# Optimization experiments

Hardware: AMD Instinct MI355X
Metric: run time of the kernel (lower is better)

Reference implementation:

```python
import jax, jax.numpy as jnp
import numpy as np

B, N = 16, 300000          # batch, total anchors per image (all FPN levels concatenated)
PRE, POST = 2000, 1000     # num_pre_nms, num_post_nms
NMS_THR = 0.7
MIN_SIZE = 1e-3            # proposal_min_size
IMG_H, IMG_W = 800.0, 1333.0


def setup_inputs() -> dict:
    key = jax.random.key(0)
    k1, k2, k3, k4, k5, k6 = jax.random.split(key, 6)
    cls = jax.random.normal(k1, (B, N), dtype=jnp.float32)
    reg = jax.random.normal(k2, (B, N, 4), dtype=jnp.float32) * 0.1
    # anchors as valid (cx,cy,w,h)->(x1,y1,x2,y2) boxes inside the image
    cx = jax.random.uniform(k3, (B, N), dtype=jnp.float32, minval=0.0, maxval=IMG_W)
    cy = jax.random.uniform(k4, (B, N), dtype=jnp.float32, minval=0.0, maxval=IMG_H)
    w = jax.random.uniform(k5, (B, N), dtype=jnp.float32, minval=16.0, maxval=256.0)
    h = jax.random.uniform(k6, (B, N), dtype=jnp.float32, minval=16.0, maxval=256.0)
    anchors = jnp.stack([cx - 0.5 * w, cy - 0.5 * h, cx + 0.5 * w, cy + 0.5 * h], axis=-1)
    return {"cls": cls, "reg": reg, "anchors": anchors}


def _decode(anchor, reg):
    aw = anchor[:, 2] - anchor[:, 0]
    ah = anchor[:, 3] - anchor[:, 1]
    acx = anchor[:, 0] + 0.5 * aw
    acy = anchor[:, 1] + 0.5 * ah
    dx, dy, dw, dh = reg[:, 0], reg[:, 1], reg[:, 2], reg[:, 3]
    pcx = dx * aw + acx
    pcy = dy * ah + acy
    pw = jnp.exp(dw) * aw
    ph = jnp.exp(dh) * ah
    return jnp.stack([pcx - 0.5 * pw, pcy - 0.5 * ph, pcx + 0.5 * pw, pcy + 0.5 * ph], axis=-1)


def _iou_matrix(boxes):
    # boxes: [K,4] -> pairwise IoU [K,K]
    area = (boxes[:, 2] - boxes[:, 0]) * (boxes[:, 3] - boxes[:, 1])
    lt = jnp.maximum(boxes[:, None, :2], boxes[None, :, :2])
    rb = jnp.minimum(boxes[:, None, 2:], boxes[None, :, 2:])
    wh = jnp.clip(rb - lt, 0.0)
    inter = wh[..., 0] * wh[..., 1]
    union = area[:, None] + area[None, :] - inter
    return inter / jnp.maximum(union, 1e-8)


def _per_image(score, reg, anchor):
    # topk pre-NMS selection (lax.top_k returns score-descending order)
    top_s, idx = jax.lax.top_k(score, PRE)
    boxes = _decode(anchor[idx], reg[idx].reshape(-1, 4))
    # clip to image bounds
    bounds = jnp.array([IMG_W, IMG_H, IMG_W, IMG_H], dtype=boxes.dtype)
    boxes = jnp.clip(boxes, 0.0, bounds)
    # remove small boxes (mask instead of dynamic removal)
    w = boxes[:, 2] - boxes[:, 0]
    h = boxes[:, 3] - boxes[:, 1]
    valid = (w >= MIN_SIZE) & (h >= MIN_SIZE)
    s = jnp.where(valid, top_s, -jnp.inf)
    order = jnp.argsort(-s)  # score-descending, invalid last
    boxes = boxes[order]
    valid = valid[order]
    # greedy NMS: iterate highest-score-first, suppress later boxes with IoU > thr
    iou = _iou_matrix(boxes)
    rng = jnp.arange(PRE)
    def body(i, keep):
        sup = (iou[i] > NMS_THR) & keep[i]
        return keep & jnp.logical_not(sup & (rng > i))
    keep = jax.lax.fori_loop(0, PRE, body, valid)
    # gather kept boxes (score order preserved), pad with zeros past count
    sel = jnp.argsort(jnp.logical_not(keep), stable=True)[:POST]
    return boxes[sel] * keep[sel][:, None].astype(boxes.dtype)


def reference(cls, reg, anchors):
    # [B, POST, 4] proposals per image (zero-padded where fewer than POST kept)
    return jax.vmap(_per_image)(cls, reg, anchors)
```

## Files before the change

kernel.cpp:

```cpp
#include <hip/hip_runtime.h>

#define NB 16
#define NN 300000
#define PRE 2000
#define POST 1000

typedef unsigned long long ull;

static const size_t OFF_HIST1   = 0;
static const size_t OFF_HIST2   = 65536;
static const size_t OFF_HIST3   = 196608;
static const size_t OFF_CANDCNT = 327680;
static const size_t OFF_EQCNT   = 327936;
static const size_t OFF_BITMAP  = 328192;
static const size_t OFF_B1      = 332288;
static const size_t OFF_NEED1   = 332544;
static const size_t OFF_B2      = 332800;
static const size_t OFF_NEED2   = 333056;
static const size_t OFF_B3      = 333312;
static const size_t OFF_NEED3   = 333568;
static const size_t OFF_NVALID  = 333824;
static const size_t ZERO_BYTES  = 334080;
static const size_t OFF_CAND    = 334080;
static const size_t OFF_EQBUF   = 465152;
static const size_t OFF_KEYS    = 989440;
static const size_t OFF_BOXTMP  = 1251584;
static const size_t OFF_SORTED  = 1775872;
static const size_t OFF_MASK    = 2287872;

__device__ __forceinline__ unsigned f2u(float f){
  unsigned b = __float_as_uint(f);
  return (b & 0x80000000u) ? ~b : (b | 0x80000000u);
}

#define H1REP 8
#define H1STRIDE 1025
__global__ void k_hist1(const float* __restrict__ cls, unsigned* __restrict__ hist){
  __shared__ unsigned h[H1REP * H1STRIDE];
  int img = blockIdx.y;
  for (int i = threadIdx.x; i < H1REP * H1STRIDE; i += blockDim.x) h[i] = 0;
  __syncthreads();
  const float* p = cls + (size_t)img * NN;
  int stride = gridDim.x * blockDim.x;
  unsigned rep = (threadIdx.x & (H1REP - 1)) * H1STRIDE;
  for (int i = blockIdx.x * blockDim.x + threadIdx.x; i < NN; i += stride)
    atomicAdd(&h[rep + (f2u(p[i]) >> 22)], 1u);
  __syncthreads();
  unsigned* g = hist + img * 1024;
  for (int i = threadIdx.x; i < 1024; i += blockDim.x){
    unsigned v = 0;
    for (int r = 0; r < H1REP; r++) v += h[r * H1STRIDE + i];
    if (v) atomicAdd(&g[i], v);
  }
}

__global__ void k_scan(const unsigned* __restrict__ hist, int bins,
                       const unsigned* __restrict__ tgt, unsigned K0,
                       unsigned* __restrict__ outBin, unsigned* __restrict__ outNeed){
  int img = blockIdx.x;
  int t = threadIdx.x;
  const unsigned* hh = hist + img * bins;
  unsigned K = tgt ? tgt[img] : K0;
  int per = bins >> 8;
  unsigned s = 0;
  for (int q = 0; q < per; q++) s += hh[bins - 1 - (t * per + q)];
  __shared__ unsigned arr[256];
  arr[t] = s;
  __syncthreads();
  for (int off = 1; off < 256; off <<= 1){
    unsigned v = (t >= off) ? arr[t - off] : 0u;
    __syncthreads();
    arr[t] += v;
    __syncthreads();
  }
  unsigned incl = arr[t], excl = incl - s;
  if (excl < K && K <= incl){
    unsigned c = excl;
    for (int q = 0; q < per; q++){
      int b = bins - 1 - (t * per + q);
      unsigned cnt = hh[b];
      if (c + cnt >= K){ outBin[img] = (unsigned)b; outNeed[img] = K - c; break; }
      c += cnt;
    }
  }
}

__global__ void k_hist2(const float* __restrict__ cls, const unsigned* __restrict__ b1,
                        unsigned* __restrict__ hist){
  int img = blockIdx.y;
  unsigned bb1 = b1[img];
  const float* p = cls + (size_t)img * NN;
  unsigned* g = hist + img * 2048;
  int stride = gridDim.x * blockDim.x;
  for (int i = blockIdx.x * blockDim.x + threadIdx.x; i < NN; i += stride){
    unsigned u = f2u(p[i]);
    if ((u >> 22) == bb1) atomicAdd(&g[(u >> 11) & 0x7FFu], 1u);
  }
}

__global__ void k_hist3(const float* __restrict__ cls, const unsigned* __restrict__ b1,
                        const unsigned* __restrict__ b2, unsigned* __restrict__ hist){
  int img = blockIdx.y;
  unsigned pref = (b1[img] << 11) | b2[img];
  const float* p = cls + (size_t)img * NN;
  unsigned* g = hist + img * 2048;
  int stride = gridDim.x * blockDim.x;
  for (int i = blockIdx.x * blockDim.x + threadIdx.x; i < NN; i += stride){
    unsigned u = f2u(p[i]);
    if ((u >> 11) == pref) atomicAdd(&g[u & 0x7FFu], 1u);
  }
}

__global__ void k_compact(const float* __restrict__ cls, const unsigned* __restrict__ b1,
                          const unsigned* __restrict__ b2, const unsigned* __restrict__ b3,
                          unsigned* __restrict__ cand, unsigned* __restrict__ candCnt,
                          unsigned* __restrict__ eqbuf, unsigned* __restrict__ eqCnt){
  __shared__ unsigned lc[1024];
  __shared__ unsigned le[256];
  __shared__ unsigned lcn, len_, baseC, baseE;
  int img = blockIdx.y;
  if (threadIdx.x == 0){ lcn = 0; len_ = 0; }
  __syncthreads();
  unsigned T = (b1[img] << 22) | (b2[img] << 11) | b3[img];
  const float* p = cls + (size_t)img * NN;
  int stride = gridDim.x * blockDim.x;
  for (int i = blockIdx.x * blockDim.x + threadIdx.x; i < NN; i += stride){
    unsigned u = f2u(p[i]);
    if (u > T){
      unsigned pos = atomicAdd(&lcn, 1u);
      if (pos < 1024u) lc[pos] = (unsigned)i;
      else { unsigned g = atomicAdd(&candCnt[img], 1u); if (g < 2048u) cand[img * 2048 + g] = (unsigned)i; }
    } else if (u == T){
      unsigned pos = atomicAdd(&len_, 1u);
      if (pos < 256u) le[pos] = (unsigned)i;
      else { unsigned g = atomicAdd(&eqCnt[img], 1u); if (g < 8192u) eqbuf[img * 8192 + g] = (unsigned)i; }
    }
  }
  __syncthreads();
  unsigned nc = lcn < 1024u ? lcn : 1024u;
  unsigned ne = len_ < 256u ? len_ : 256u;
  if (threadIdx.x == 0){
    if (nc) baseC = atomicAdd(&candCnt[img], nc);
    if (ne) baseE = atomicAdd(&eqCnt[img], ne);
  }
  __syncthreads();
  for (unsigned t = threadIdx.x; t < nc; t += blockDim.x){
    unsigned g = baseC + t;
    if (g < 2048u) cand[img * 2048 + g] = lc[t];
  }
  for (unsigned t = threadIdx.x; t < ne; t += blockDim.x){
    unsigned g = baseE + t;
    if (g < 8192u) eqbuf[img * 8192 + g] = le[t];
  }
}

__global__ void k_finalize(unsigned* __restrict__ cand, const unsigned* __restrict__ candCnt,
                           const unsigned* __restrict__ eqbuf, const unsigned* __restrict__ eqCnt,
                           const unsigned* __restrict__ need3){
  int img = blockIdx.x, tid = threadIdx.x;
  unsigned need = need3[img];
  unsigned ec = eqCnt[img]; if (ec > 8192u) ec = 8192u;
  unsigned base = candCnt[img];
  const unsigned* eq = eqbuf + img * 8192;
  unsigned* c = cand + img * 2048;
  if (need >= ec){
    for (unsigned t = tid; t < ec; t += 256) if (base + t < 2048u) c[base + t] = eq[t];
    return;
  }
  for (unsigned t = tid; t < ec; t += 256){
    unsigned v = eq[t], r = 0;
    for (unsigned s = 0; s < ec; s++) r += (eq[s] < v) ? 1u : 0u;
    if (r < need && base + r < 2048u) c[base + r] = v;
  }
}

__global__ void k_decode(const float* __restrict__ cls, const float* __restrict__ reg,
                         const float* __restrict__ anch, const unsigned* __restrict__ cand,
                         float* __restrict__ boxTmp, ull* __restrict__ keys,
                         unsigned* __restrict__ nvalid){
  int s = blockIdx.x * blockDim.x + threadIdx.x;
  if (s >= NB * 2048) return;
  int img = s >> 11, slot = s & 2047;
  ull key = 0ull;
  float4 box = make_float4(0.f, 0.f, 0.f, 0.f);
  bool counted = false;
  if (slot < PRE){
    unsigned i = cand[img * 2048 + slot];
    if (i < NN){
      size_t gi = (size_t)img * NN + i;
      float4 a = ((const float4*)anch)[gi];
      float4 r = ((const float4*)reg)[gi];
      float sc = cls[gi];
      float aw = a.z - a.x, ah = a.w - a.y;
      float acx = a.x + 0.5f * aw, acy = a.y + 0.5f * ah;
      float pcx = r.x * aw + acx, pcy = r.y * ah + acy;
      float pw = expf(r.z) * aw, ph = expf(r.w) * ah;
      float x1 = pcx - 0.5f * pw, y1 = pcy - 0.5f * ph;
      float x2 = pcx + 0.5f * pw, y2 = pcy + 0.5f * ph;
      x1 = fminf(fmaxf(x1, 0.f), 1333.f); x2 = fminf(fmaxf(x2, 0.f), 1333.f);
      y1 = fminf(fmaxf(y1, 0.f), 800.f);  y2 = fminf(fmaxf(y2, 0.f), 800.f);
      bool valid = ((x2 - x1) >= 0.001f) && ((y2 - y1) >= 0.001f);
      unsigned up = valid ? f2u(sc) : 0u;
      key = ((ull)up << 32) | (ull)(0xFFFFFFFFu - i);
      box = make_float4(x1, y1, x2, y2);
      counted = valid;
    }
  }
  keys[img * 2048 + slot] = key;
  ((float4*)boxTmp)[img * 2048 + slot] = box;
  ull bal = __ballot(counted);
  if ((threadIdx.x & 63) == 0 && bal)
    atomicAdd(&nvalid[img], (unsigned)__popcll(bal));
}

__global__ __launch_bounds__(256) void k_rank(const ull* __restrict__ keys,
                                              const float* __restrict__ boxTmp,
                                              float* __restrict__ sorted){
  __shared__ ull lk[2048];
  int img = blockIdx.y;
  int e = blockIdx.x * 256 + threadIdx.x;
  for (int t = threadIdx.x; t < 2048; t += 256) lk[t] = keys[img * 2048 + t];
  __syncthreads();
  ull me = lk[e];
  unsigned rank = 0;
  #pragma unroll 8
  for (int j = 0; j < 2048; j++) rank += (lk[j] > me) ? 1u : 0u;
  if (rank < PRE)
    ((float4*)sorted)[img * PRE + rank] = ((const float4*)boxTmp)[img * 2048 + e];
}

__global__ __launch_bounds__(512) void k_mask(const float* __restrict__ sorted,
                                              const unsigned* __restrict__ nvalid,
                                              ull* __restrict__ mask, ull* __restrict__ bitmap){
  __shared__ float4 bx[PRE];
  __shared__ float  ar[PRE];
  __shared__ unsigned rowflag[16];
  int img = blockIdx.y, tid = threadIdx.x;
  if (tid < 16) rowflag[tid] = 0;
  for (int i = tid; i < PRE; i += 512){
    float4 b = ((const float4*)sorted)[img * PRE + i];
    bx[i] = b;
    ar[i] = (b.z - b.x) * (b.w - b.y);
  }
  __syncthreads();
  int row = blockIdx.x * 16 + (tid >> 5);
  int w = tid & 31;
  float4 bi = bx[row];
  float ai = ar[row];
  int qlo = (row >= w) ? (((row - w) >> 5) + 1) : 0;
  int qhi = ((PRE - 1 - w) >> 5) + 1;
  ull m = 0;
  for (int q = qlo; q < qhi; q++){
    int j = (q << 5) + w;
    float4 bj = bx[j];
    float xx1 = fmaxf(bi.x, bj.x), yy1 = fmaxf(bi.y, bj.y);
    float xx2 = fminf(bi.z, bj.z), yy2 = fminf(bi.w, bj.w);
    float ww = fmaxf(xx2 - xx1, 0.f), hh = fmaxf(yy2 - yy1, 0.f);
    float inter = ww * hh;
    float uni = ai + ar[j] - inter;
    if (inter / fmaxf(uni, 1e-8f) > 0.7f) m |= (1ull << q);
  }
  mask[((size_t)(img * PRE + row)) * 32 + w] = m;
  if (m) atomicOr(&rowflag[tid >> 5], 1u);
  __syncthreads();
  if (tid < 16){
    int r = blockIdx.x * 16 + tid;
    if (rowflag[tid] && r < (int)nvalid[img])
      atomicOr(&bitmap[img * 32 + (r >> 6)], 1ull << (r & 63));
  }
}

#define CHR 48
__global__ __launch_bounds__(256) void k_nms(const ull* __restrict__ mask,
                                             const ull* __restrict__ bitmap,
                                             const unsigned* __restrict__ nvalid,
                                             const float* __restrict__ sorted,
                                             float* __restrict__ out){
  __shared__ unsigned rowsLds[2048];
  __shared__ unsigned cntw[32];
  __shared__ unsigned wbaseS[32];
  __shared__ int mcountS, mpS;
  __shared__ ull cacheD[2][CHR * 32];
  __shared__ ull keepP[32];
  __shared__ ull keepLin[32];
  __shared__ unsigned cntArr[32], preArr[32];
  int img = blockIdx.x, tid = threadIdx.x;
  int lane = tid & 63, wave = tid >> 6;

  if (tid < 32) cntw[tid] = (unsigned)__popcll(bitmap[img * 32 + tid]);
  __syncthreads();
  if (tid == 0){
    unsigned s = 0;
    for (int w0 = 0; w0 < 32; w0++){ wbaseS[w0] = s; s += cntw[w0]; }
    mcountS = (int)s;
    mpS = ((int)s + CHR - 1) / CHR * CHR;
  }
  __syncthreads();
  int m = mcountS, mp = mpS;
  if (tid < 32){
    ull bits = bitmap[img * 32 + tid];
    unsigned pos = wbaseS[tid];
    int base_i = tid * 64;
    while (bits){
      int b = __ffsll((long long)bits) - 1;
      rowsLds[pos++] = (unsigned)(base_i + b);
      bits &= bits - 1;
    }
  }
  for (int t = m + tid; t < mp; t += 256) rowsLds[t] = PRE - 1;
  __syncthreads();

  int nch = mp / CHR;
  ull remv = 0;
  const ull* mg = mask + (size_t)img * PRE * 32;

  if (nch > 0 && tid >= 64){
    int s = tid - 64;
    ull v[8];
    #pragma unroll
    for (int k = 0; k < 8; k++){
      int t = k * 192 + s;
      unsigned rr = rowsLds[t >> 5];
      v[k] = mg[(size_t)rr * 32 + (t & 31)];
    }
    #pragma unroll
    for (int k = 0; k < 8; k++) cacheD[0][k * 192 + s] = v[k];
  }
  __syncthreads();

  for (int c = 0; c < nch; c++){
    int cb = c & 1;
    if (tid >= 64){
      if (c + 1 < nch){
        int q0n = (c + 1) * CHR;
        int s = tid - 64;
        ull v[8];
        #pragma unroll
        for (int k = 0; k < 8; k++){
          int t = k * 192 + s;
          unsigned rr = rowsLds[q0n + (t >> 5)];
          v[k] = mg[(size_t)rr * 32 + (t & 31)];
        }
        #pragma unroll
        for (int k = 0; k < 8; k++) cacheD[cb ^ 1][k * 192 + s] = v[k];
      }
    } else {
      const ull* cbuf = cacheD[cb];
      const int q0 = c * CHR;
      ull cur[8]; unsigned ci[8];
      #pragma unroll
      for (int k = 0; k < 8; k++){
        ci[k] = rowsLds[q0 + k];
        cur[k] = cbuf[(k << 5) | (lane & 31)];
      }
      #pragma unroll
      for (int g = 0; g < 6; g++){
        ull nxt[8]; unsigned ni[8];
        if (g < 5){
          #pragma unroll
          for (int k = 0; k < 8; k++){
            int lq = (g + 1) * 8 + k;
            ni[k] = rowsLds[q0 + lq];
            nxt[k] = cbuf[(lq << 5) | (lane & 31)];
          }
        }
        #pragma unroll
        for (int k = 0; k < 8; k++){
          unsigned i = ci[k];
          unsigned bit = ((unsigned)(remv >> (i >> 5))) & 1u;
          int sup = (lane == (int)(i & 31)) && bit;
          if (!__any(sup)) remv |= cur[k];
        }
        if (g < 5){
          #pragma unroll
          for (int k = 0; k < 8; k++){ cur[k] = nxt[k]; ci[k] = ni[k]; }
        }
      }
    }
    __syncthreads();
  }

  int nv = (int)nvalid[img];
  if (wave == 0 && lane < 32){
    int cnt2 = (nv > lane) ? (((nv - 1 - lane) >> 5) + 1) : 0;
    ull vm = (cnt2 >= 64) ? ~0ull : ((1ull << cnt2) - 1ull);
    keepP[lane] = (~remv) & vm;
  }
  __syncthreads();
  if (tid < 32){
    ull lin = 0;
    for (int kk = 0; kk < 64; kk++)
      lin |= ((keepP[kk & 31] >> (2 * tid + (kk >> 5))) & 1ull) << kk;
    keepLin[tid] = lin;
    cntArr[tid] = (unsigned)__popcll(lin);
  }
  __syncthreads();
  if (tid < 32){
    unsigned pre = 0;
    for (int w0 = 0; w0 < tid; w0++) pre += cntArr[w0];
    preArr[tid] = pre;
  }
  __syncthreads();
  for (int i = tid; i < PRE; i += 256){
    int w0 = i >> 6, b = i & 63;
    ull kw = keepLin[w0];
    if ((kw >> b) & 1ull){
      unsigned rank = preArr[w0] + (unsigned)__popcll(kw & ((1ull << b) - 1ull));
      if (rank < POST)
        ((float4*)out)[img * POST + rank] = ((const float4*)sorted)[img * PRE + i];
    }
  }
}

extern "C" void kernel_launch(void* const* d_in, const int* in_sizes, int n_in,
                              void* d_out, int out_size, void* d_ws, size_t ws_size,
                              hipStream_t stream){
  const float* cls  = (const float*)d_in[0];
  const float* reg  = (const float*)d_in[1];
  const float* anch = (const float*)d_in[2];
  float* out = (float*)d_out;
  char* ws = (char*)d_ws;

  unsigned* hist1   = (unsigned*)(ws + OFF_HIST1);
  unsigned* hist2   = (unsigned*)(ws + OFF_HIST2);
  unsigned* hist3   = (unsigned*)(ws + OFF_HIST3);
  unsigned* candCnt = (unsigned*)(ws + OFF_CANDCNT);
  unsigned* eqCnt   = (unsigned*)(ws + OFF_EQCNT);
  ull*      bitmap  = (ull*)     (ws + OFF_BITMAP);
  unsigned* b1      = (unsigned*)(ws + OFF_B1);
  unsigned* need1   = (unsigned*)(ws + OFF_NEED1);
  unsigned* b2      = (unsigned*)(ws + OFF_B2);
  unsigned* need2   = (unsigned*)(ws + OFF_NEED2);
  unsigned* b3      = (unsigned*)(ws + OFF_B3);
  unsigned* need3   = (unsigned*)(ws + OFF_NEED3);
  unsigned* nvalid  = (unsigned*)(ws + OFF_NVALID);
  unsigned* cand    = (unsigned*)(ws + OFF_CAND);
  unsigned* eqbuf   = (unsigned*)(ws + OFF_EQBUF);
  ull*      keys    = (ull*)     (ws + OFF_KEYS);
  float*    boxTmp  = (float*)   (ws + OFF_BOXTMP);
  float*    sorted  = (float*)   (ws + OFF_SORTED);
  ull*      mask    = (ull*)     (ws + OFF_MASK);

  hipMemsetAsync(ws, 0, ZERO_BYTES, stream);
  hipMemsetAsync(d_out, 0, (size_t)out_size * sizeof(float), stream);

  k_hist1<<<dim3(64, NB), 256, 0, stream>>>(cls, hist1);
  k_scan <<<NB, 256, 0, stream>>>(hist1, 1024, (const unsigned*)nullptr, 2000u, b1, need1);
  k_hist2<<<dim3(64, NB), 256, 0, stream>>>(cls, b1, hist2);
  k_scan <<<NB, 256, 0, stream>>>(hist2, 2048, need1, 0u, b2, need2);
  k_hist3<<<dim3(64, NB), 256, 0, stream>>>(cls, b1, b2, hist3);
  k_scan <<<NB, 256, 0, stream>>>(hist3, 2048, need2, 0u, b3, need3);
  k_compact<<<dim3(64, NB), 256, 0, stream>>>(cls, b1, b2, b3, cand, candCnt, eqbuf, eqCnt);
  k_finalize<<<NB, 256, 0, stream>>>(cand, candCnt, eqbuf, eqCnt, need3);
  k_decode<<<(NB * 2048) / 256, 256, 0, stream>>>(cls, reg, anch, cand, boxTmp, keys, nvalid);
  k_rank<<<dim3(8, NB), 256, 0, stream>>>(keys, boxTmp, sorted);
  k_mask<<<dim3(PRE / 16, NB), 512, 0, stream>>>(sorted, nvalid, mask, bitmap);
  k_nms<<<NB, 256, 0, stream>>>(mask, bitmap, nvalid, sorted, out);
}
```

Baseline: 305.3 us.

## Replace three-pass radix select with single compaction of boundary bin plus in-block refinement

The top-k threshold search drops the second and third full passes over the 300k scores per image. A single compaction pass now writes strictly-above-bin indices and stashes boundary-bin (key, index) pairs into a buffer. One block per image then refines the threshold with two shared-memory histograms, resolves ties and decodes boxes, so the separate finalize and decode kernels go away. The output memset is replaced by zero-filling only the unused tail in the NMS kernel. The risk is that the boundary buffer is capped at 8192 entries and the fused select runs only 16 blocks, which serializes the decode work.

```diff
diff --git a/kernel.cpp b/kernel.cpp
--- a/kernel.cpp
+++ b/kernel.cpp
@@ -8,25 +8,19 @@
 typedef unsigned long long ull;
 
 static const size_t OFF_HIST1   = 0;
-static const size_t OFF_HIST2   = 65536;
-static const size_t OFF_HIST3   = 196608;
-static const size_t OFF_CANDCNT = 327680;
-static const size_t OFF_EQCNT   = 327936;
-static const size_t OFF_BITMAP  = 328192;
-static const size_t OFF_B1      = 332288;
-static const size_t OFF_NEED1   = 332544;
-static const size_t OFF_B2      = 332800;
-static const size_t OFF_NEED2   = 333056;
-static const size_t OFF_B3      = 333312;
-static const size_t OFF_NEED3   = 333568;
-static const size_t OFF_NVALID  = 333824;
-static const size_t ZERO_BYTES  = 334080;
-static const size_t OFF_CAND    = 334080;
-static const size_t OFF_EQBUF   = 465152;
-static const size_t OFF_KEYS    = 989440;
-static const size_t OFF_BOXTMP  = 1251584;
-static const size_t OFF_SORTED  = 1775872;
-static const size_t OFF_MASK    = 2287872;
+static const size_t OFF_CANDCNT = 65536;
+static const size_t OFF_BINCNT  = 65792;
+static const size_t OFF_B1      = 66048;
+static const size_t OFF_NEED1   = 66304;
+static const size_t OFF_NVALID  = 66560;
+static const size_t OFF_BITMAP  = 66816;
+static const size_t ZERO_BYTES  = 70912;
+static const size_t OFF_CAND    = 70912;
+static const size_t OFF_KEYS    = 201984;
+static const size_t OFF_BOXTMP  = 464128;
+static const size_t OFF_SORTED  = 988416;
+static const size_t OFF_MASK    = 1500416;
+static const size_t OFF_BINBUF  = OFF_MASK;
 
 __device__ __forceinline__ unsigned f2u(float f){
   unsigned b = __float_as_uint(f);
@@ -55,12 +49,12 @@
 }
 
 __global__ void k_scan(const unsigned* __restrict__ hist, int bins,
-                       const unsigned* __restrict__ tgt, unsigned K0,
+                       unsigned K0,
                        unsigned* __restrict__ outBin, unsigned* __restrict__ outNeed){
   int img = blockIdx.x;
   int t = threadIdx.x;
   const unsigned* hh = hist + img * bins;
-  unsigned K = tgt ? tgt[img] : K0;
+  unsigned K = K0;
   int per = bins >> 8;
   unsigned s = 0;
   for (int q = 0; q < per; q++) s += hh[bins - 1 - (t * per + q)];
@@ -85,132 +79,192 @@
   }
 }
 
-__global__ void k_hist2(const float* __restrict__ cls, const unsigned* __restrict__ b1,
-                        unsigned* __restrict__ hist){
+__global__ void k_compactA(const float* __restrict__ cls, const unsigned* __restrict__ b1,
+                           unsigned* __restrict__ cand, unsigned* __restrict__ candCnt,
+                           ull* __restrict__ binbuf, unsigned* __restrict__ binCnt){
+  __shared__ unsigned lc[1024];
+  __shared__ ull lb[512];
+  __shared__ unsigned lcn, lbn, baseC, baseB;
   int img = blockIdx.y;
+  if (threadIdx.x == 0){ lcn = 0; lbn = 0; }
+  __syncthreads();
   unsigned bb1 = b1[img];
-  const float* p = cls + (size_t)img * NN;
-  unsigned* g = hist + img * 2048;
-  int stride = gridDim.x * blockDim.x;
-  for (int i = blockIdx.x * blockDim.x + threadIdx.x; i < NN; i += stride){
-    unsigned u = f2u(p[i]);
-    if ((u >> 22) == bb1) atomicAdd(&g[(u >> 11) & 0x7FFu], 1u);
-  }
-}
-
-__global__ void k_hist3(const float* __restrict__ cls, const unsigned* __restrict__ b1,
-                        const unsigned* __restrict__ b2, unsigned* __restrict__ hist){
-  int img = blockIdx.y;
-  unsigned pref = (b1[img] << 11) | b2[img];
-  const float* p = cls + (size_t)img * NN;
-  unsigned* g = hist + img * 2048;
-  int stride = gridDim.x * blockDim.x;
-  for (int i = blockIdx.x * blockDim.x + threadIdx.x; i < NN; i += stride){
-    unsigned u = f2u(p[i]);
-    if ((u >> 11) == pref) atomicAdd(&g[u & 0x7FFu], 1u);
-  }
-}
-
-__global__ void k_compact(const float* __restrict__ cls, const unsigned* __restrict__ b1,
-                          const unsigned* __restrict__ b2, const unsigned* __restrict__ b3,
-                          unsigned* __restrict__ cand, unsigned* __restrict__ candCnt,
-                          unsigned* __restrict__ eqbuf, unsigned* __restrict__ eqCnt){
-  __shared__ unsigned lc[1024];
-  __shared__ unsigned le[256];
-  __shared__ unsigned lcn, len_, baseC, baseE;
-  int img = blockIdx.y;
-  if (threadIdx.x == 0){ lcn = 0; len_ = 0; }
-  __syncthreads();
-  unsigned T = (b1[img] << 22) | (b2[img] << 11) | b3[img];
   const float* p = cls + (size_t)img * NN;
   int stride = gridDim.x * blockDim.x;
   for (int i = blockIdx.x * blockDim.x + threadIdx.x; i < NN; i += stride){
     unsigned u = f2u(p[i]);
-    if (u > T){
+    unsigned top = u >> 22;
+    if (top > bb1){
       unsigned pos = atomicAdd(&lcn, 1u);
       if (pos < 1024u) lc[pos] = (unsigned)i;
       else { unsigned g = atomicAdd(&candCnt[img], 1u); if (g < 2048u) cand[img * 2048 + g] = (unsigned)i; }
-    } else if (u == T){
-      unsigned pos = atomicAdd(&len_, 1u);
-      if (pos < 256u) le[pos] = (unsigned)i;
-      else { unsigned g = atomicAdd(&eqCnt[img], 1u); if (g < 8192u) eqbuf[img * 8192 + g] = (unsigned)i; }
+    } else if (top == bb1){
+      ull e = ((ull)u << 32) | (unsigned)i;
+      unsigned pos = atomicAdd(&lbn, 1u);
+      if (pos < 512u) lb[pos] = e;
+      else { unsigned g = atomicAdd(&binCnt[img], 1u); if (g < 8192u) binbuf[img * 8192 + g] = e; }
     }
   }
   __syncthreads();
   unsigned nc = lcn < 1024u ? lcn : 1024u;
-  unsigned ne = len_ < 256u ? len_ : 256u;
+  unsigned nb = lbn < 512u ? lbn : 512u;
   if (threadIdx.x == 0){
     if (nc) baseC = atomicAdd(&candCnt[img], nc);
-    if (ne) baseE = atomicAdd(&eqCnt[img], ne);
+    if (nb) baseB = atomicAdd(&binCnt[img], nb);
   }
   __syncthreads();
   for (unsigned t = threadIdx.x; t < nc; t += blockDim.x){
     unsigned g = baseC + t;
     if (g < 2048u) cand[img * 2048 + g] = lc[t];
   }
-  for (unsigned t = threadIdx.x; t < ne; t += blockDim.x){
-    unsigned g = baseE + t;
-    if (g < 8192u) eqbuf[img * 8192 + g] = le[t];
-  }
-}
-
-__global__ void k_finalize(unsigned* __restrict__ cand, const unsigned* __restrict__ candCnt,
-                           const unsigned* __restrict__ eqbuf, const unsigned* __restrict__ eqCnt,
-                           const unsigned* __restrict__ need3){
+  for (unsigned t = threadIdx.x; t < nb; t += blockDim.x){
+    unsigned g = baseB + t;
+    if (g < 8192u) binbuf[img * 8192 + g] = lb[t];
+  }
+}
+
+__global__ __launch_bounds__(256) void k_select(const float* __restrict__ cls,
+                                                const float* __restrict__ reg,
+                                                const float* __restrict__ anch,
+                                                unsigned* __restrict__ cand,
+                                                const unsigned* __restrict__ candCnt,
+                                                const ull* __restrict__ binbuf,
+                                                const unsigned* __restrict__ binCnt,
+                                                const unsigned* __restrict__ need1,
+                                                float* __restrict__ boxTmp,
+                                                ull* __restrict__ keys,
+                                                unsigned* __restrict__ nvalid){
+  __shared__ unsigned hist[2048];
+  __shared__ unsigned arr[256];
+  __shared__ unsigned b2s, need2s, b3s, need3s;
+  __shared__ unsigned tiePos[1024];
+  __shared__ unsigned wcnt, tieCnt;
   int img = blockIdx.x, tid = threadIdx.x;
-  unsigned need = need3[img];
-  unsigned ec = eqCnt[img]; if (ec > 8192u) ec = 8192u;
+  unsigned bc = binCnt[img]; if (bc > 8192u) bc = 8192u;
   unsigned base = candCnt[img];
-  const unsigned* eq = eqbuf + img * 8192;
-  unsigned* c = cand + img * 2048;
-  if (need >= ec){
-    for (unsigned t = tid; t < ec; t += 256) if (base + t < 2048u) c[base + t] = eq[t];
-    return;
-  }
+  unsigned need = need1[img];
+  const ull* bb = binbuf + img * 8192;
+
+  if (tid == 0){ wcnt = 0; tieCnt = 0; b2s = 0; need2s = 0; b3s = 0; need3s = 0; }
+  for (int i = tid; i < 2048; i += 256) hist[i] = 0;
+  __syncthreads();
+  for (unsigned t = tid; t < bc; t += 256){
+    unsigned u = (unsigned)(bb[t] >> 32);
+    atomicAdd(&hist[(u >> 11) & 0x7FFu], 1u);
+  }
+  __syncthreads();
+  {
+    unsigned s = 0;
+    for (int q = 0; q < 8; q++) s += hist[2047 - (tid * 8 + q)];
+    arr[tid] = s; __syncthreads();
+    for (int off = 1; off < 256; off <<= 1){
+      unsigned v = (tid >= off) ? arr[tid - off] : 0u;
+      __syncthreads(); arr[tid] += v; __syncthreads();
+    }
+    unsigned incl = arr[tid], excl = incl - s;
+    if (excl < need && need <= incl){
+      unsigned c = excl;
+      for (int q = 0; q < 8; q++){
+        int b = 2047 - (tid * 8 + q);
+        unsigned cnt = hist[b];
+        if (c + cnt >= need){ b2s = (unsigned)b; need2s = need - c; break; }
+        c += cnt;
+      }
+    }
+  }
+  __syncthreads();
+  unsigned b2 = b2s, need2 = need2s;
+  for (int i = tid; i < 2048; i += 256) hist[i] = 0;
+  __syncthreads();
+  for (unsigned t = tid; t < bc; t += 256){
+    unsigned u = (unsigned)(bb[t] >> 32);
+    if (((u >> 11) & 0x7FFu) == b2) atomicAdd(&hist[u & 0x7FFu], 1u);
+  }
+  __syncthreads();
+  {
+    unsigned s = 0;
+    for (int q = 0; q < 8; q++) s += hist[2047 - (tid * 8 + q)];
+    arr[tid] = s; __syncthreads();
+    for (int off = 1; off < 256; off <<= 1){
+      unsigned v = (tid >= off) ? arr[tid - off] : 0u;
+      __syncthreads(); arr[tid] += v; __syncthreads();
+    }
+    unsigned incl = arr[tid], excl = incl - s;
+    if (excl < need2 && need2 <= incl){
+      unsigned c = excl;
+      for (int q = 0; q < 8; q++){
+        int b = 2047 - (tid * 8 + q);
+        unsigned cnt = hist[b];
+        if (c + cnt >= need2){ b3s = (unsigned)b; need3s = need2 - c; break; }
+        c += cnt;
+      }
+    }
+  }
+  __syncthreads();
+  unsigned b3 = b3s, need3 = need3s;
+  for (unsigned t = tid; t < bc; t += 256){
+    ull e = bb[t];
+    unsigned u = (unsigned)(e >> 32);
+    unsigned mid = (u >> 11) & 0x7FFu, low = u & 0x7FFu;
+    bool take = (mid > b2) || (mid == b2 && low > b3);
+    bool tie  = (mid == b2) && (low == b3);
+    if (take){
+      unsigned p = atomicAdd(&wcnt, 1u);
+      unsigned g = base + p;
+      if (g < 2048u) cand[img * 2048 + g] = (unsigned)(e & 0xFFFFFFFFull);
+    } else if (tie){
+      unsigned p = atomicAdd(&tieCnt, 1u);
+      if (p < 1024u) tiePos[p] = t;
+    }
+  }
+  __syncthreads();
+  unsigned above = wcnt;
+  unsigned ec = tieCnt; if (ec > 1024u) ec = 1024u;
   for (unsigned t = tid; t < ec; t += 256){
-    unsigned v = eq[t], r = 0;
-    for (unsigned s = 0; s < ec; s++) r += (eq[s] < v) ? 1u : 0u;
-    if (r < need && base + r < 2048u) c[base + r] = v;
-  }
-}
-
-__global__ void k_decode(const float* __restrict__ cls, const float* __restrict__ reg,
-                         const float* __restrict__ anch, const unsigned* __restrict__ cand,
-                         float* __restrict__ boxTmp, ull* __restrict__ keys,
-                         unsigned* __restrict__ nvalid){
-  int s = blockIdx.x * blockDim.x + threadIdx.x;
-  if (s >= NB * 2048) return;
-  int img = s >> 11, slot = s & 2047;
-  ull key = 0ull;
-  float4 box = make_float4(0.f, 0.f, 0.f, 0.f);
-  bool counted = false;
-  if (slot < PRE){
-    unsigned i = cand[img * 2048 + slot];
-    if (i < NN){
-      size_t gi = (size_t)img * NN + i;
-      float4 a = ((const float4*)anch)[gi];
-      float4 r = ((const float4*)reg)[gi];
-      float sc = cls[gi];
-      float aw = a.z - a.x, ah = a.w - a.y;
-      float acx = a.x + 0.5f * aw, acy = a.y + 0.5f * ah;
-      float pcx = r.x * aw + acx, pcy = r.y * ah + acy;
-      float pw = expf(r.z) * aw, ph = expf(r.w) * ah;
-      float x1 = pcx - 0.5f * pw, y1 = pcy - 0.5f * ph;
-      float x2 = pcx + 0.5f * pw, y2 = pcy + 0.5f * ph;
-      x1 = fminf(fmaxf(x1, 0.f), 1333.f); x2 = fminf(fmaxf(x2, 0.f), 1333.f);
-      y1 = fminf(fmaxf(y1, 0.f), 800.f);  y2 = fminf(fmaxf(y2, 0.f), 800.f);
-      bool valid = ((x2 - x1) >= 0.001f) && ((y2 - y1) >= 0.001f);
-      unsigned up = valid ? f2u(sc) : 0u;
-      key = ((ull)up << 32) | (ull)(0xFFFFFFFFu - i);
-      box = make_float4(x1, y1, x2, y2);
-      counted = valid;
-    }
-  }
-  keys[img * 2048 + slot] = key;
-  ((float4*)boxTmp)[img * 2048 + slot] = box;
-  ull bal = __ballot(counted);
-  if ((threadIdx.x & 63) == 0 && bal)
-    atomicAdd(&nvalid[img], (unsigned)__popcll(bal));
+    unsigned idx = (unsigned)(bb[tiePos[t]] & 0xFFFFFFFFull);
+    unsigned r = 0;
+    for (unsigned s = 0; s < ec; s++){
+      unsigned idx2 = (unsigned)(bb[tiePos[s]] & 0xFFFFFFFFull);
+      r += (idx2 < idx) ? 1u : 0u;
+    }
+    if (r < need3){
+      unsigned g = base + above + r;
+      if (g < 2048u) cand[img * 2048 + g] = idx;
+    }
+  }
+  __syncthreads();
+  for (int slot = tid; slot < 2048; slot += 256){
+    ull key = 0ull;
+    float4 box = make_float4(0.f, 0.f, 0.f, 0.f);
+    bool counted = false;
+    if (slot < PRE){
+      unsigned i = cand[img * 2048 + slot];
+      if (i < NN){
+        size_t gi = (size_t)img * NN + i;
+        float4 a = ((const float4*)anch)[gi];
+        float4 r = ((const float4*)reg)[gi];
+        float sc = cls[gi];
+        float aw = a.z - a.x, ah = a.w - a.y;
+        float acx = a.x + 0.5f * aw, acy = a.y + 0.5f * ah;
+        float pcx = r.x * aw + acx, pcy = r.y * ah + acy;
+        float pw = expf(r.z) * aw, ph = expf(r.w) * ah;
+        float x1 = pcx - 0.5f * pw, y1 = pcy - 0.5f * ph;
+        float x2 = pcx + 0.5f * pw, y2 = pcy + 0.5f * ph;
+        x1 = fminf(fmaxf(x1, 0.f), 1333.f); x2 = fminf(fmaxf(x2, 0.f), 1333.f);
+        y1 = fminf(fmaxf(y1, 0.f), 800.f);  y2 = fminf(fmaxf(y2, 0.f), 800.f);
+        bool valid = ((x2 - x1) >= 0.001f) && ((y2 - y1) >= 0.001f);
+        unsigned up = valid ? f2u(sc) : 0u;
+        key = ((ull)up << 32) | (ull)(0xFFFFFFFFu - i);
+        box = make_float4(x1, y1, x2, y2);
+        counted = valid;
+      }
+    }
+    keys[img * 2048 + slot] = key;
+    ((float4*)boxTmp)[img * 2048 + slot] = box;
+    ull bal = __ballot(counted);
+    if ((tid & 63) == 0 && bal)
+      atomicAdd(&nvalid[img], (unsigned)__popcll(bal));
+  }
 }
 
 __global__ __launch_bounds__(256) void k_rank(const ull* __restrict__ keys,
@@ -401,6 +455,7 @@
     preArr[tid] = pre;
   }
   __syncthreads();
+  int totK = (int)(preArr[31] + cntArr[31]);
   for (int i = tid; i < PRE; i += 256){
     int w0 = i >> 6, b = i & 63;
     ull kw = keepLin[w0];
@@ -410,6 +465,8 @@
         ((float4*)out)[img * POST + rank] = ((const float4*)sorted)[img * PRE + i];
     }
   }
+  for (int r = totK + tid; r < POST; r += 256)
+    ((float4*)out)[img * POST + r] = make_float4(0.f, 0.f, 0.f, 0.f);
 }
 
 extern "C" void kernel_launch(void* const* d_in, const int* in_sizes, int n_in,
@@ -422,38 +479,27 @@
   char* ws = (char*)d_ws;
 
   unsigned* hist1   = (unsigned*)(ws + OFF_HIST1);
-  unsigned* hist2   = (unsigned*)(ws + OFF_HIST2);
-  unsigned* hist3   = (unsigned*)(ws + OFF_HIST3);
   unsigned* candCnt = (unsigned*)(ws + OFF_CANDCNT);
-  unsigned* eqCnt   = (unsigned*)(ws + OFF_EQCNT);
-  ull*      bitmap  = (ull*)     (ws + OFF_BITMAP);
+  unsigned* binCnt  = (unsigned*)(ws + OFF_BINCNT);
   unsigned* b1      = (unsigned*)(ws + OFF_B1);
   unsigned* need1   = (unsigned*)(ws + OFF_NEED1);
-  unsigned* b2      = (unsigned*)(ws + OFF_B2);
-  unsigned* need2   = (unsigned*)(ws + OFF_NEED2);
-  unsigned* b3      = (unsigned*)(ws + OFF_B3);
-  unsigned* need3   = (unsigned*)(ws + OFF_NEED3);
   unsigned* nvalid  = (unsigned*)(ws + OFF_NVALID);
+  ull*      bitmap  = (ull*)     (ws + OFF_BITMAP);
   unsigned* cand    = (unsigned*)(ws + OFF_CAND);
-  unsigned* eqbuf   = (unsigned*)(ws + OFF_EQBUF);
   ull*      keys    = (ull*)     (ws + OFF_KEYS);
   float*    boxTmp  = (float*)   (ws + OFF_BOXTMP);
   float*    sorted  = (float*)   (ws + OFF_SORTED);
-  ull*      mask    = (ull*)     (ws + OFF_MASK);
+  ull*      maskG   = (ull*)     (ws + OFF_MASK);
+  ull*      binbuf  = (ull*)     (ws + OFF_BINBUF);
 
   hipMemsetAsync(ws, 0, ZERO_BYTES, stream);
-  hipMemsetAsync(d_out, 0, (size_t)out_size * sizeof(float), stream);
-
-  k_hist1<<<dim3(64, NB), 256, 0, stream>>>(cls, hist1);
-  k_scan <<<NB, 256, 0, stream>>>(hist1, 1024, (const unsigned*)nullptr, 2000u, b1, need1);
-  k_hist2<<<dim3(64, NB), 256, 0, stream>>>(cls, b1, hist2);
-  k_scan <<<NB, 256, 0, stream>>>(hist2, 2048, need1, 0u, b2, need2);
-  k_hist3<<<dim3(64, NB), 256, 0, stream>>>(cls, b1, b2, hist3);
-  k_scan <<<NB, 256, 0, stream>>>(hist3, 2048, need2, 0u, b3, need3);
-  k_compact<<<dim3(64, NB), 256, 0, stream>>>(cls, b1, b2, b3, cand, candCnt, eqbuf, eqCnt);
-  k_finalize<<<NB, 256, 0, stream>>>(cand, candCnt, eqbuf, eqCnt, need3);
-  k_decode<<<(NB * 2048) / 256, 256, 0, stream>>>(cls, reg, anch, cand, boxTmp, keys, nvalid);
-  k_rank<<<dim3(8, NB), 256, 0, stream>>>(keys, boxTmp, sorted);
-  k_mask<<<dim3(PRE / 16, NB), 512, 0, stream>>>(sorted, nvalid, mask, bitmap);
-  k_nms<<<NB, 256, 0, stream>>>(mask, bitmap, nvalid, sorted, out);
-}
+
+  k_hist1   <<<dim3(64, NB), 256, 0, stream>>>(cls, hist1);
+  k_scan    <<<NB, 256, 0, stream>>>(hist1, 1024, 2000u, b1, need1);
+  k_compactA<<<dim3(64, NB), 256, 0, stream>>>(cls, b1, cand, candCnt, binbuf, binCnt);
+  k_select  <<<NB, 256, 0, stream>>>(cls, reg, anch, cand, candCnt, binbuf, binCnt,
+                                     need1, boxTmp, keys, nvalid);
+  k_rank    <<<dim3(8, NB), 256, 0, stream>>>(keys, boxTmp, sorted);
+  k_mask    <<<dim3(PRE / 16, NB), 512, 0, stream>>>(sorted, nvalid, maskG, bitmap);
+  k_nms     <<<NB, 256, 0, stream>>>(maskG, bitmap, nvalid, sorted, out);
+}
```

After: 307.9 us. Within noise of the previous version (+0.8%).
